# Kernel tuning notes

Hardware: AMD Instinct MI355X
Metric: run time of the kernel (lower is better)

The kernel has to match this reference:

```python
import jax, jax.numpy as jnp
import numpy as np

H, A, V = 8, 32, 32
NODE_IN, EDGE_IN, NODE_OUT, EDGE_OUT = 128, 64, 128, 64


def setup_inputs() -> dict:
    key = jax.random.key(0)
    ks = jax.random.split(key, 8)
    B, N = 1, 384
    s = lambda fan: 1.0 / np.sqrt(fan).astype(np.float32)
    nodes = jax.random.normal(ks[0], (B, NODE_IN, N), jnp.float32)
    edges = jax.random.normal(ks[1], (B, EDGE_IN, N, N), jnp.float32)
    mask = jax.random.randint(ks[2], (B, N), 0, 2).astype(bool)
    W_q = jax.random.normal(ks[3], (A * H, NODE_IN), jnp.float32) * s(NODE_IN)
    W_k = jax.random.normal(ks[4], (A * H, NODE_IN + EDGE_IN), jnp.float32) * s(NODE_IN + EDGE_IN)
    W_v = jax.random.normal(ks[5], (V * H, NODE_IN + EDGE_IN), jnp.float32) * s(NODE_IN + EDGE_IN)
    W_o = jax.random.normal(ks[6], (NODE_OUT, V * H), jnp.float32) * s(V * H)
    W_e = jax.random.normal(ks[7], (EDGE_OUT, V * H + EDGE_IN), jnp.float32) * s(V * H + EDGE_IN)
    return dict(nodes=nodes, edges=edges, mask=mask, W_q=W_q, W_k=W_k, W_v=W_v, W_o=W_o, W_e=W_e)


def reference(nodes, edges, mask, W_q, W_k, W_v, W_o, W_e):
    B, C, N = nodes.shape
    # 1x1 convs are channel matmuls
    query = jnp.einsum('oc,bcn->bon', W_q, nodes)                      # [B, H*A, N]
    node_edges = jnp.concatenate(
        [jnp.broadcast_to(nodes[:, :, :, None], (B, C, N, N)), edges], axis=1)  # [B, C+E, N, N]
    key = jnp.einsum('oc,bcij->boij', W_k, node_edges)                 # [B, H*A, N, N]
    value = jnp.einsum('oc,bcij->boij', W_v, node_edges).reshape(B, H, V, N, N)
    # elementwise QK: query broadcast over column axis j
    sim = (query[:, :, :, None] * key).reshape(B, H, A, N, N).sum(axis=2)
    sim = sim / jnp.sqrt(jnp.asarray(A, sim.dtype))                    # [B, H, N, N]
    sim = jnp.where(mask[:, None, None, :], sim, -jnp.inf)
    sim = jax.nn.softmax(sim, axis=-1)
    mm = (mask[:, None, :, None] & mask[:, None, None, :]).astype(sim.dtype)  # [B,1,N,N]
    sim = sim * mm
    value = value * mm[:, None]
    node_features = jnp.einsum('bhij,bhvij->bhvi', sim, value).reshape(B, H * V, N)
    node_out = jnp.einsum('od,bdn->bon', W_o, node_features)           # [B, node_out, N]
    # symmetrized edge features: (f_i + f_j) / 2, then concat raw edges
    ef = (node_features[:, :, :, None] + node_features[:, :, None, :]) * 0.5  # [B,H*V,N,N]
    ef = jnp.concatenate([ef, edges], axis=1)
    edge_out = jnp.einsum('oc,bcij->boij', W_e, ef)                    # [B, edge_out, N, N]
    return node_out, edge_out
```

## Files before the change

### kernel.cpp

```cpp
#include <hip/hip_runtime.h>
#include <math.h>

#define NN 384
#define NSQ (NN*NN)

#define WS_MASKF 0
#define WS_C1    384
#define WS_P     3456
#define WS_VN    200064
#define WS_T     298368
#define WS_GH    494976
#define WS_WT    519552

__global__ __launch_bounds__(256) void k_proj(
    const float* __restrict__ nodes, const float* __restrict__ Wq,
    const float* __restrict__ Wk, const float* __restrict__ Wv,
    const float* __restrict__ We, const unsigned int* __restrict__ mi,
    float* __restrict__ ws) {
    int tid = threadIdx.x;
    if (blockIdx.x == 48) {
        __shared__ int bytemode;
        if (tid == 0) bytemode = 0;
        __syncthreads();
        unsigned v0 = mi[tid];
        unsigned v1 = (tid < 128) ? mi[256 + tid] : 0u;
        if (v0 > 1u || v1 > 1u) bytemode = 1;
        __syncthreads();
        float* maskf = ws + WS_MASKF;
        for (int j = tid; j < NN; j += 256) {
            int on;
            if (bytemode) on = (((const unsigned char*)mi)[j] != 0);
            else          on = (mi[j] != 0u);
            maskf[j] = on ? 1.0f : 0.0f;
        }
        return;
    }
    if (blockIdx.x == 49) {
        float* Wt = ws + WS_WT;
        for (int idx = tid; idx < 4096; idx += 256) {
            int c = idx >> 6, o = idx & 63;
            Wt[c * 64 + o] = We[o * 320 + 256 + c];
        }
        return;
    }
    float* c1_ws = ws + WS_C1;
    float* P_ws  = ws + WS_P;
    float* vn_ws = ws + WS_VN;
    int i0 = blockIdx.x * 8;
    __shared__ float nl[128][8];
    __shared__ float q_l[256][8];
    __shared__ float qk_l[256][8];
    for (int idx = tid; idx < 1024; idx += 256) {
        int m = idx >> 3, ii = idx & 7;
        nl[m][ii] = nodes[m * NN + i0 + ii];
    }
    __syncthreads();
    int o = tid;
    float aq[8], ak[8], av[8];
#pragma unroll
    for (int ii = 0; ii < 8; ii++) { aq[ii] = 0.f; ak[ii] = 0.f; av[ii] = 0.f; }
#pragma unroll 4
    for (int m = 0; m < 128; m++) {
        float wq = Wq[o * 128 + m];
        float wk = Wk[o * 192 + m];
        float wv = Wv[o * 192 + m];
#pragma unroll
        for (int ii = 0; ii < 8; ii++) {
            float nv = nl[m][ii];
            aq[ii] = fmaf(wq, nv, aq[ii]);
            ak[ii] = fmaf(wk, nv, ak[ii]);
            av[ii] = fmaf(wv, nv, av[ii]);
        }
    }
#pragma unroll
    for (int ii = 0; ii < 8; ii++) {
        vn_ws[(size_t)(i0 + ii) * 256 + o] = av[ii];
        q_l[o][ii]  = aq[ii];
        qk_l[o][ii] = aq[ii] * ak[ii];
    }
    __syncthreads();
    if (tid < 64) {
        int h = tid >> 3, ii = tid & 7;
        float s = 0.f;
        for (int a = 0; a < 32; a++) s += qk_l[h * 32 + a][ii];
        c1_ws[(i0 + ii) * 8 + h] = s;
    }
    for (int rep = 0; rep < 2; rep++) {
        int idx = rep * 256 + tid;
        int c = idx & 63, h = idx >> 6;
        float ap[8];
#pragma unroll
        for (int ii = 0; ii < 8; ii++) ap[ii] = 0.f;
        for (int a = 0; a < 32; a++) {
            float w = Wk[(h * 32 + a) * 192 + 128 + c];
#pragma unroll
            for (int ii = 0; ii < 8; ii++)
                ap[ii] = fmaf(q_l[h * 32 + a][ii], w, ap[ii]);
        }
#pragma unroll
        for (int ii = 0; ii < 8; ii++)
            P_ws[(size_t)(i0 + ii) * 512 + c * 8 + h] = ap[ii];
    }
}

__global__ __launch_bounds__(512) void k_attn(
    const float* __restrict__ edges, const float* __restrict__ ws_ro,
    float* __restrict__ T_ws) {
    __shared__ __align__(16) unsigned short epad_h[64 * 390];
    __shared__ __align__(16) float sT2[NN * 8];
    const float* maskf = ws_ro + WS_MASKF;
    const float* c1w   = ws_ro + WS_C1;
    const float* Pw    = ws_ro + WS_P;
    int i = blockIdx.x;
    int tid = threadIdx.x;
    int wv = tid >> 6, ln = tid & 63;
    float mask_i = maskf[i];

    if (tid < NN) {
        int j = tid;
        const float* eb = edges + (size_t)i * NN + j;
        const float* Pi = Pw + (size_t)i * 512;
        float acc[8];
#pragma unroll
        for (int h = 0; h < 8; h++) acc[h] = 0.f;
#pragma unroll
        for (int cb = 0; cb < 4; cb++) {
            float ev[16];
#pragma unroll
            for (int t = 0; t < 16; t++)
                ev[t] = eb[(size_t)(cb * 16 + t) * NSQ];
#pragma unroll
            for (int t = 0; t < 16; t++) {
                int c = cb * 16 + t;
                unsigned u = __float_as_uint(ev[t]);
                epad_h[c * 390 + j] =
                    (unsigned short)((u + 0x7FFFu + ((u >> 16) & 1u)) >> 16);
                const float* Pc = Pi + c * 8;
#pragma unroll
                for (int h = 0; h < 8; h++) acc[h] = fmaf(Pc[h], ev[t], acc[h]);
            }
        }
        float mj = maskf[j];
        const float* c1i = c1w + i * 8;
        float sv[8];
#pragma unroll
        for (int h = 0; h < 8; h++) {
            float s = (c1i[h] + acc[h]) * 0.17677669529663687f;
            sv[h] = (mj != 0.0f) ? s : -1e30f;
        }
        *reinterpret_cast<float4*>(&sT2[j * 8])     = make_float4(sv[0], sv[1], sv[2], sv[3]);
        *reinterpret_cast<float4*>(&sT2[j * 8 + 4]) = make_float4(sv[4], sv[5], sv[6], sv[7]);
    }
    __syncthreads();
    {
        int h = wv;
        float v[6];
#pragma unroll
        for (int k = 0; k < 6; k++) v[k] = sT2[(ln + 64 * k) * 8 + h];
        float m = v[0];
#pragma unroll
        for (int k = 1; k < 6; k++) m = fmaxf(m, v[k]);
#pragma unroll
        for (int s = 1; s < 64; s <<= 1) m = fmaxf(m, __shfl_xor(m, s));
        float ex[6]; float sum = 0.f;
#pragma unroll
        for (int k = 0; k < 6; k++) { ex[k] = __expf(v[k] - m); sum += ex[k]; }
#pragma unroll
        for (int s = 1; s < 64; s <<= 1) sum += __shfl_xor(sum, s);
        float fac = mask_i / sum;
#pragma unroll
        for (int k = 0; k < 6; k++) sT2[(ln + 64 * k) * 8 + h] = ex[k] * fac;
    }
    __syncthreads();
    float t[8];
#pragma unroll
    for (int h = 0; h < 8; h++) t[h] = 0.f;
    {
        int c = ln;
        int j0 = wv * 48;
        for (int j = j0; j < j0 + 48; j++) {
            float e = __uint_as_float(((unsigned)epad_h[c * 390 + j]) << 16);
            float4 s0 = *reinterpret_cast<const float4*>(&sT2[j * 8]);
            float4 s1 = *reinterpret_cast<const float4*>(&sT2[j * 8 + 4]);
            t[0] = fmaf(s0.x, e, t[0]); t[1] = fmaf(s0.y, e, t[1]);
            t[2] = fmaf(s0.z, e, t[2]); t[3] = fmaf(s0.w, e, t[3]);
            t[4] = fmaf(s1.x, e, t[4]); t[5] = fmaf(s1.y, e, t[5]);
            t[6] = fmaf(s1.z, e, t[6]); t[7] = fmaf(s1.w, e, t[7]);
        }
    }
    __syncthreads();
    float* Tp = reinterpret_cast<float*>(epad_h);
#pragma unroll
    for (int h = 0; h < 8; h++) Tp[wv * 512 + h * 64 + ln] = t[h];
    __syncthreads();
    {
        int h = tid >> 6, c = tid & 63;
        float s = 0.f;
#pragma unroll
        for (int w = 0; w < 8; w++) s += Tp[w * 512 + h * 64 + c];
        T_ws[(size_t)i * 512 + h * 64 + c] = s;
    }
}

__global__ __launch_bounds__(256) void k_nf(
    const float* __restrict__ Wv, const float* __restrict__ Wo,
    const float* __restrict__ We, const float* __restrict__ ws_ro,
    float* __restrict__ gh_ws, float* __restrict__ out) {
    const float* maskf = ws_ro + WS_MASKF;
    const float* vn_ws = ws_ro + WS_VN;
    const float* T_ws  = ws_ro + WS_T;
    int i = blockIdx.x, tid = threadIdx.x;
    __shared__ float T_l[512];
    __shared__ float nf_l[256];
    T_l[tid]       = T_ws[(size_t)i * 512 + tid];
    T_l[tid + 256] = T_ws[(size_t)i * 512 + 256 + tid];
    __syncthreads();
    int d = tid, h = d >> 5;
    float a0 = 0.f, a1 = 0.f, a2 = 0.f, a3 = 0.f;
#pragma unroll
    for (int c = 0; c < 64; c += 4) {
        a0 = fmaf(Wv[d * 192 + 128 + c],     T_l[h * 64 + c],     a0);
        a1 = fmaf(Wv[d * 192 + 128 + c + 1], T_l[h * 64 + c + 1], a1);
        a2 = fmaf(Wv[d * 192 + 128 + c + 2], T_l[h * 64 + c + 2], a2);
        a3 = fmaf(Wv[d * 192 + 128 + c + 3], T_l[h * 64 + c + 3], a3);
    }
    nf_l[d] = maskf[i] * vn_ws[(size_t)i * 256 + d] + ((a0 + a1) + (a2 + a3));
    __syncthreads();
    if (tid < 128) {
        int o = tid;
        float b0 = 0.f, b1 = 0.f, b2 = 0.f, b3 = 0.f;
#pragma unroll 8
        for (int dd = 0; dd < 256; dd += 4) {
            b0 = fmaf(Wo[o * 256 + dd],     nf_l[dd],     b0);
            b1 = fmaf(Wo[o * 256 + dd + 1], nf_l[dd + 1], b1);
            b2 = fmaf(Wo[o * 256 + dd + 2], nf_l[dd + 2], b2);
            b3 = fmaf(Wo[o * 256 + dd + 3], nf_l[dd + 3], b3);
        }
        out[o * NN + i] = (b0 + b1) + (b2 + b3);
    } else if (tid < 192) {
        int o = tid - 128;
        float b0 = 0.f, b1 = 0.f, b2 = 0.f, b3 = 0.f;
#pragma unroll 8
        for (int dd = 0; dd < 256; dd += 4) {
            b0 = fmaf(We[o * 320 + dd],     nf_l[dd],     b0);
            b1 = fmaf(We[o * 320 + dd + 1], nf_l[dd + 1], b1);
            b2 = fmaf(We[o * 320 + dd + 2], nf_l[dd + 2], b2);
            b3 = fmaf(We[o * 320 + dd + 3], nf_l[dd + 3], b3);
        }
        gh_ws[o * NN + i] = 0.5f * ((b0 + b1) + (b2 + b3));
    }
}

__global__ __launch_bounds__(384) void k_edge(
    const float* __restrict__ edges, const float* __restrict__ ws_ro,
    float* __restrict__ out_e) {
    const float* Wt = ws_ro + WS_WT;
    const float* gh = ws_ro + WS_GH;
    int i = blockIdx.x, og = blockIdx.y, j = threadIdx.x;
    float gj[16];
    const float* gb = gh + og * 16 * NN + j;
#pragma unroll
    for (int t = 0; t < 16; t++) gj[t] = gb[t * NN];
    float eo[16];
#pragma unroll
    for (int t = 0; t < 16; t++) eo[t] = 0.f;
    const float* eb = edges + (size_t)i * NN + j;
    const float* wtb = Wt + og * 16;
#pragma unroll 4
    for (int c = 0; c < 64; c++) {
        float e = eb[(size_t)c * NSQ];
        const float* wr = wtb + c * 64;
#pragma unroll
        for (int t = 0; t < 16; t++) eo[t] = fmaf(wr[t], e, eo[t]);
    }
    size_t ob = (size_t)i * NN + j;
    const float* gib = gh + og * 16 * NN + i;
#pragma unroll
    for (int t = 0; t < 16; t++) {
        float gi = gib[t * NN];
        out_e[(size_t)(og * 16 + t) * NSQ + ob] = eo[t] + gi + gj[t];
    }
}

extern "C" void kernel_launch(void* const* d_in, const int* in_sizes, int n_in,
                              void* d_out, int out_size, void* d_ws, size_t ws_size,
                              hipStream_t stream) {
    const float* nodes = (const float*)d_in[0];
    const float* edges = (const float*)d_in[1];
    const unsigned int* mask = (const unsigned int*)d_in[2];
    const float* Wq = (const float*)d_in[3];
    const float* Wk = (const float*)d_in[4];
    const float* Wv = (const float*)d_in[5];
    const float* Wo = (const float*)d_in[6];
    const float* We = (const float*)d_in[7];
    float* out = (float*)d_out;
    float* ws  = (float*)d_ws;
    float* out_e = out + 128 * NN;

    hipLaunchKernelGGL(k_proj, dim3(50), dim3(256), 0, stream,
                       nodes, Wq, Wk, Wv, We, mask, ws);
    hipLaunchKernelGGL(k_attn, dim3(384), dim3(512), 0, stream,
                       edges, ws, ws + WS_T);
    hipLaunchKernelGGL(k_nf, dim3(384), dim3(256), 0, stream, Wv, Wo, We, ws,
                       ws + WS_GH, out);
    hipLaunchKernelGGL(k_edge, dim3(384, 4), dim3(384), 0, stream,
                       edges, ws, out_e);
}
```

Measured before the change: 176.8 us.

## Use bf16 MFMA for attention-edge reduction and pre-transpose weights for coalescing

The per-row softmax-weighted reduction over edges in k_attn moves from scalar FMAs across 8 waves to bf16 MFMA 16x16x32 instructions run by a single wave. The softmax weights are also stored as bf16, and the LDS pitch changes to 392 so the 16-byte vector loads stay aligned. Extra k_proj blocks pre-transpose Wo, the edge part of Wv, and the node part of We, so the weight reads in k_nf are coalesced. k_edge now batches 16 edge-channel loads before its FMAs to get more memory parallelism. The costs are lower precision in the attention weights and only one active wave doing the MFMA stage.

```diff
diff --git a/kernel.cpp b/kernel.cpp
--- a/kernel.cpp
+++ b/kernel.cpp
@@ -11,35 +11,64 @@
 #define WS_T     298368
 #define WS_GH    494976
 #define WS_WT    519552
+#define WS_WOT   523648
+#define WS_WVE   556416
+#define WS_WEN   572800
+
+typedef short short8 __attribute__((ext_vector_type(8)));
+typedef float f32x4 __attribute__((ext_vector_type(4)));
+
+__device__ __forceinline__ unsigned short f2bf(float x) {
+    unsigned u = __float_as_uint(x);
+    return (unsigned short)((u + 0x7FFFu + ((u >> 16) & 1u)) >> 16);
+}
 
 __global__ __launch_bounds__(256) void k_proj(
     const float* __restrict__ nodes, const float* __restrict__ Wq,
     const float* __restrict__ Wk, const float* __restrict__ Wv,
-    const float* __restrict__ We, const unsigned int* __restrict__ mi,
-    float* __restrict__ ws) {
+    const float* __restrict__ Wo, const float* __restrict__ We,
+    const unsigned int* __restrict__ mi, float* __restrict__ ws) {
     int tid = threadIdx.x;
-    if (blockIdx.x == 48) {
-        __shared__ int bytemode;
-        if (tid == 0) bytemode = 0;
-        __syncthreads();
-        unsigned v0 = mi[tid];
-        unsigned v1 = (tid < 128) ? mi[256 + tid] : 0u;
-        if (v0 > 1u || v1 > 1u) bytemode = 1;
-        __syncthreads();
-        float* maskf = ws + WS_MASKF;
-        for (int j = tid; j < NN; j += 256) {
-            int on;
-            if (bytemode) on = (((const unsigned char*)mi)[j] != 0);
-            else          on = (mi[j] != 0u);
-            maskf[j] = on ? 1.0f : 0.0f;
-        }
-        return;
-    }
-    if (blockIdx.x == 49) {
-        float* Wt = ws + WS_WT;
-        for (int idx = tid; idx < 4096; idx += 256) {
-            int c = idx >> 6, o = idx & 63;
-            Wt[c * 64 + o] = We[o * 320 + 256 + c];
+    if (blockIdx.x >= 48) {
+        if (blockIdx.x == 48) {
+            __shared__ int bytemode;
+            if (tid == 0) bytemode = 0;
+            __syncthreads();
+            unsigned v0 = mi[tid];
+            unsigned v1 = (tid < 128) ? mi[256 + tid] : 0u;
+            if (v0 > 1u || v1 > 1u) bytemode = 1;
+            __syncthreads();
+            float* maskf = ws + WS_MASKF;
+            for (int j = tid; j < NN; j += 256) {
+                int on;
+                if (bytemode) on = (((const unsigned char*)mi)[j] != 0);
+                else          on = (mi[j] != 0u);
+                maskf[j] = on ? 1.0f : 0.0f;
+            }
+        } else if (blockIdx.x == 49) {
+            float* Wt = ws + WS_WT;
+            for (int idx = tid; idx < 4096; idx += 256) {
+                int c = idx >> 6, o = idx & 63;
+                Wt[c * 64 + o] = We[o * 320 + 256 + c];
+            }
+        } else if (blockIdx.x == 50) {
+            float* WoT = ws + WS_WOT;
+            for (int idx = tid; idx < 32768; idx += 256) {
+                int dd = idx >> 7, o = idx & 127;
+                WoT[dd * 128 + o] = Wo[o * 256 + dd];
+            }
+        } else if (blockIdx.x == 51) {
+            float* WvE = ws + WS_WVE;
+            for (int idx = tid; idx < 16384; idx += 256) {
+                int c = idx >> 8, d = idx & 255;
+                WvE[c * 256 + d] = Wv[d * 192 + 128 + c];
+            }
+        } else {
+            float* WeN = ws + WS_WEN;
+            for (int idx = tid; idx < 16384; idx += 256) {
+                int dd = idx >> 6, o = idx & 63;
+                WeN[dd * 64 + o] = We[o * 320 + dd];
+            }
         }
         return;
     }
@@ -106,7 +135,7 @@
 __global__ __launch_bounds__(512) void k_attn(
     const float* __restrict__ edges, const float* __restrict__ ws_ro,
     float* __restrict__ T_ws) {
-    __shared__ __align__(16) unsigned short epad_h[64 * 390];
+    __shared__ __align__(16) unsigned short epad_h[64 * 392];
     __shared__ __align__(16) float sT2[NN * 8];
     const float* maskf = ws_ro + WS_MASKF;
     const float* c1w   = ws_ro + WS_C1;
@@ -132,9 +161,7 @@
 #pragma unroll
             for (int t = 0; t < 16; t++) {
                 int c = cb * 16 + t;
-                unsigned u = __float_as_uint(ev[t]);
-                epad_h[c * 390 + j] =
-                    (unsigned short)((u + 0x7FFFu + ((u >> 16) & 1u)) >> 16);
+                epad_h[c * 392 + j] = f2bf(ev[t]);
                 const float* Pc = Pi + c * 8;
 #pragma unroll
                 for (int h = 0; h < 8; h++) acc[h] = fmaf(Pc[h], ev[t], acc[h]);
@@ -152,11 +179,15 @@
         *reinterpret_cast<float4*>(&sT2[j * 8 + 4]) = make_float4(sv[4], sv[5], sv[6], sv[7]);
     }
     __syncthreads();
+    float v[6];
     {
         int h = wv;
-        float v[6];
 #pragma unroll
         for (int k = 0; k < 6; k++) v[k] = sT2[(ln + 64 * k) * 8 + h];
+    }
+    __syncthreads();
+    {
+        int h = wv;
         float m = v[0];
 #pragma unroll
         for (int k = 1; k < 6; k++) m = fmaxf(m, v[k]);
@@ -168,47 +199,58 @@
 #pragma unroll
         for (int s = 1; s < 64; s <<= 1) sum += __shfl_xor(sum, s);
         float fac = mask_i / sum;
-#pragma unroll
-        for (int k = 0; k < 6; k++) sT2[(ln + 64 * k) * 8 + h] = ex[k] * fac;
-    }
-    __syncthreads();
-    float t[8];
-#pragma unroll
-    for (int h = 0; h < 8; h++) t[h] = 0.f;
-    {
-        int c = ln;
-        int j0 = wv * 48;
-        for (int j = j0; j < j0 + 48; j++) {
-            float e = __uint_as_float(((unsigned)epad_h[c * 390 + j]) << 16);
-            float4 s0 = *reinterpret_cast<const float4*>(&sT2[j * 8]);
-            float4 s1 = *reinterpret_cast<const float4*>(&sT2[j * 8 + 4]);
-            t[0] = fmaf(s0.x, e, t[0]); t[1] = fmaf(s0.y, e, t[1]);
-            t[2] = fmaf(s0.z, e, t[2]); t[3] = fmaf(s0.w, e, t[3]);
-            t[4] = fmaf(s1.x, e, t[4]); t[5] = fmaf(s1.y, e, t[5]);
-            t[6] = fmaf(s1.z, e, t[6]); t[7] = fmaf(s1.w, e, t[7]);
-        }
-    }
-    __syncthreads();
-    float* Tp = reinterpret_cast<float*>(epad_h);
-#pragma unroll
-    for (int h = 0; h < 8; h++) Tp[wv * 512 + h * 64 + ln] = t[h];
-    __syncthreads();
-    {
-        int h = tid >> 6, c = tid & 63;
-        float s = 0.f;
-#pragma unroll
-        for (int w = 0; w < 8; w++) s += Tp[w * 512 + h * 64 + c];
-        T_ws[(size_t)i * 512 + h * 64 + c] = s;
+        unsigned short* s_bf = reinterpret_cast<unsigned short*>(sT2);
+#pragma unroll
+        for (int k = 0; k < 6; k++)
+            s_bf[h * 392 + ln + 64 * k] = f2bf(ex[k] * fac);
+    }
+    __syncthreads();
+    if (tid < 64) {
+        const unsigned short* s_bf = reinterpret_cast<const unsigned short*>(sT2);
+        int L = tid;
+        int nc   = L & 15;
+        int quad = L >> 4;
+        int hrow = nc & 7;
+        f32x4 acc0 = {0.f, 0.f, 0.f, 0.f};
+        f32x4 acc1 = {0.f, 0.f, 0.f, 0.f};
+        f32x4 acc2 = {0.f, 0.f, 0.f, 0.f};
+        f32x4 acc3 = {0.f, 0.f, 0.f, 0.f};
+#pragma unroll
+        for (int s = 0; s < 12; s++) {
+            int jb = s * 32 + quad * 8;
+            short8 a = *reinterpret_cast<const short8*>(&s_bf[hrow * 392 + jb]);
+            short8 b0 = *reinterpret_cast<const short8*>(&epad_h[(0 * 16 + nc) * 392 + jb]);
+            short8 b1 = *reinterpret_cast<const short8*>(&epad_h[(1 * 16 + nc) * 392 + jb]);
+            short8 b2 = *reinterpret_cast<const short8*>(&epad_h[(2 * 16 + nc) * 392 + jb]);
+            short8 b3 = *reinterpret_cast<const short8*>(&epad_h[(3 * 16 + nc) * 392 + jb]);
+            acc0 = __builtin_amdgcn_mfma_f32_16x16x32_bf16(a, b0, acc0, 0, 0, 0);
+            acc1 = __builtin_amdgcn_mfma_f32_16x16x32_bf16(a, b1, acc1, 0, 0, 0);
+            acc2 = __builtin_amdgcn_mfma_f32_16x16x32_bf16(a, b2, acc2, 0, 0, 0);
+            acc3 = __builtin_amdgcn_mfma_f32_16x16x32_bf16(a, b3, acc3, 0, 0, 0);
+        }
+        if (L < 32) {
+            float* To = T_ws + (size_t)i * 512;
+#pragma unroll
+            for (int r = 0; r < 4; r++) {
+                int h = quad * 4 + r;
+                To[h * 64 +  0 + nc] = acc0[r];
+                To[h * 64 + 16 + nc] = acc1[r];
+                To[h * 64 + 32 + nc] = acc2[r];
+                To[h * 64 + 48 + nc] = acc3[r];
+            }
+        }
     }
 }
 
 __global__ __launch_bounds__(256) void k_nf(
-    const float* __restrict__ Wv, const float* __restrict__ Wo,
-    const float* __restrict__ We, const float* __restrict__ ws_ro,
-    float* __restrict__ gh_ws, float* __restrict__ out) {
+    const float* __restrict__ ws_ro, float* __restrict__ gh_ws,
+    float* __restrict__ out) {
     const float* maskf = ws_ro + WS_MASKF;
     const float* vn_ws = ws_ro + WS_VN;
     const float* T_ws  = ws_ro + WS_T;
+    const float* WvE   = ws_ro + WS_WVE;
+    const float* WoT   = ws_ro + WS_WOT;
+    const float* WeN   = ws_ro + WS_WEN;
     int i = blockIdx.x, tid = threadIdx.x;
     __shared__ float T_l[512];
     __shared__ float nf_l[256];
@@ -219,10 +261,10 @@
     float a0 = 0.f, a1 = 0.f, a2 = 0.f, a3 = 0.f;
 #pragma unroll
     for (int c = 0; c < 64; c += 4) {
-        a0 = fmaf(Wv[d * 192 + 128 + c],     T_l[h * 64 + c],     a0);
-        a1 = fmaf(Wv[d * 192 + 128 + c + 1], T_l[h * 64 + c + 1], a1);
-        a2 = fmaf(Wv[d * 192 + 128 + c + 2], T_l[h * 64 + c + 2], a2);
-        a3 = fmaf(Wv[d * 192 + 128 + c + 3], T_l[h * 64 + c + 3], a3);
+        a0 = fmaf(WvE[(c    ) * 256 + d], T_l[h * 64 + c    ], a0);
+        a1 = fmaf(WvE[(c + 1) * 256 + d], T_l[h * 64 + c + 1], a1);
+        a2 = fmaf(WvE[(c + 2) * 256 + d], T_l[h * 64 + c + 2], a2);
+        a3 = fmaf(WvE[(c + 3) * 256 + d], T_l[h * 64 + c + 3], a3);
     }
     nf_l[d] = maskf[i] * vn_ws[(size_t)i * 256 + d] + ((a0 + a1) + (a2 + a3));
     __syncthreads();
@@ -231,10 +273,10 @@
         float b0 = 0.f, b1 = 0.f, b2 = 0.f, b3 = 0.f;
 #pragma unroll 8
         for (int dd = 0; dd < 256; dd += 4) {
-            b0 = fmaf(Wo[o * 256 + dd],     nf_l[dd],     b0);
-            b1 = fmaf(Wo[o * 256 + dd + 1], nf_l[dd + 1], b1);
-            b2 = fmaf(Wo[o * 256 + dd + 2], nf_l[dd + 2], b2);
-            b3 = fmaf(Wo[o * 256 + dd + 3], nf_l[dd + 3], b3);
+            b0 = fmaf(WoT[(dd    ) * 128 + o], nf_l[dd    ], b0);
+            b1 = fmaf(WoT[(dd + 1) * 128 + o], nf_l[dd + 1], b1);
+            b2 = fmaf(WoT[(dd + 2) * 128 + o], nf_l[dd + 2], b2);
+            b3 = fmaf(WoT[(dd + 3) * 128 + o], nf_l[dd + 3], b3);
         }
         out[o * NN + i] = (b0 + b1) + (b2 + b3);
     } else if (tid < 192) {
@@ -242,10 +284,10 @@
         float b0 = 0.f, b1 = 0.f, b2 = 0.f, b3 = 0.f;
 #pragma unroll 8
         for (int dd = 0; dd < 256; dd += 4) {
-            b0 = fmaf(We[o * 320 + dd],     nf_l[dd],     b0);
-            b1 = fmaf(We[o * 320 + dd + 1], nf_l[dd + 1], b1);
-            b2 = fmaf(We[o * 320 + dd + 2], nf_l[dd + 2], b2);
-            b3 = fmaf(We[o * 320 + dd + 3], nf_l[dd + 3], b3);
+            b0 = fmaf(WeN[(dd    ) * 64 + o], nf_l[dd    ], b0);
+            b1 = fmaf(WeN[(dd + 1) * 64 + o], nf_l[dd + 1], b1);
+            b2 = fmaf(WeN[(dd + 2) * 64 + o], nf_l[dd + 2], b2);
+            b3 = fmaf(WeN[(dd + 3) * 64 + o], nf_l[dd + 3], b3);
         }
         gh_ws[o * NN + i] = 0.5f * ((b0 + b1) + (b2 + b3));
     }
@@ -266,12 +308,18 @@
     for (int t = 0; t < 16; t++) eo[t] = 0.f;
     const float* eb = edges + (size_t)i * NN + j;
     const float* wtb = Wt + og * 16;
-#pragma unroll 4
-    for (int c = 0; c < 64; c++) {
-        float e = eb[(size_t)c * NSQ];
-        const float* wr = wtb + c * 64;
-#pragma unroll
-        for (int t = 0; t < 16; t++) eo[t] = fmaf(wr[t], e, eo[t]);
+#pragma unroll
+    for (int cb = 0; cb < 4; cb++) {
+        float ev[16];
+#pragma unroll
+        for (int t = 0; t < 16; t++)
+            ev[t] = eb[(size_t)(cb * 16 + t) * NSQ];
+#pragma unroll
+        for (int t = 0; t < 16; t++) {
+            const float* wr = wtb + (cb * 16 + t) * 64;
+#pragma unroll
+            for (int u = 0; u < 16; u++) eo[u] = fmaf(wr[u], ev[t], eo[u]);
+        }
     }
     size_t ob = (size_t)i * NN + j;
     const float* gib = gh + og * 16 * NN + i;
@@ -297,11 +345,11 @@
     float* ws  = (float*)d_ws;
     float* out_e = out + 128 * NN;
 
-    hipLaunchKernelGGL(k_proj, dim3(50), dim3(256), 0, stream,
-                       nodes, Wq, Wk, Wv, We, mask, ws);
+    hipLaunchKernelGGL(k_proj, dim3(53), dim3(256), 0, stream,
+                       nodes, Wq, Wk, Wv, Wo, We, mask, ws);
     hipLaunchKernelGGL(k_attn, dim3(384), dim3(512), 0, stream,
                        edges, ws, ws + WS_T);
-    hipLaunchKernelGGL(k_nf, dim3(384), dim3(256), 0, stream, Wv, Wo, We, ws,
+    hipLaunchKernelGGL(k_nf, dim3(384), dim3(256), 0, stream, ws,
                        ws + WS_GH, out);
     hipLaunchKernelGGL(k_edge, dim3(384, 4), dim3(384), 0, stream,
                        edges, ws, out_e);
```

Result: faster. 172.4 us (-2.5%).
